# Kernel optimization log

Measured on AMD Instinct MI355X. Metric: run time of the kernel, lower is better.

Reference implementation:

```python
import jax, jax.numpy as jnp
import numpy as np

B, N_PATTS, D_PATTS, L_PATTS, L_SEQ = 32, 32, 12, 32, 1024
L_OUT = 32
RHO = 1.0
BIG = 1e30  # stands in for +inf at DP boundaries (finite to keep grads clean)


def setup_inputs() -> dict:
    key = jax.random.key(0)
    kx, kp = jax.random.split(key)
    x = jax.random.normal(kx, (B, D_PATTS, L_SEQ), dtype=jnp.float32)
    patts = jax.random.normal(kp, (N_PATTS, D_PATTS, L_PATTS), dtype=jnp.float32)
    return {"x": x, "patts": patts}


def _pairwise_sqdist(x, patts):
    # cost[b,n,i,j] = sum_d (patts[n,d,i] - x[b,d,j])^2, shape [B,N,P,L]
    x2 = jnp.sum(x * x, axis=1)            # [B,L]
    p2 = jnp.sum(patts * patts, axis=1)    # [N,P]
    cross = jnp.einsum('bdl,ndp->bnpl', x, patts)  # [B,N,P,L]
    return p2[None, :, :, None] + x2[:, None, None, :] - 2.0 * cross


def _dp_column(a, c, w):
    # Solve cur[i] = c[i] + min(a[i], w*cur[i-1]) sequentially over pattern axis.
    # a, c: [B,N,P]; returns [B,N,P]
    a_t = jnp.moveaxis(a, -1, 0)  # [P,B,N]
    c_t = jnp.moveaxis(c, -1, 0)

    def step(cur_prev, ac):
        a_i, c_i = ac
        cur = c_i + jnp.minimum(a_i, w * cur_prev)
        return cur, cur

    init = jnp.full(c.shape[:-1], BIG, c.dtype)  # no row above the first
    _, cur = jax.lax.scan(step, init, (a_t, c_t))
    return jnp.moveaxis(cur, 0, -1)


def _dtw_dp(cost, w):
    # Weighted DTW recurrence:
    #   D[i,j] = cost[i,j] + min(D[i-1,j-1], w*D[i-1,j], w*D[i,j-1])
    # with D[0,0] = cost[0,0] and out-of-range predecessors = +inf.
    # cost: [B,N,P,L] -> D: [B,N,P,L]
    Bb, Nn, P, L = cost.shape
    cost_t = jnp.moveaxis(cost, -1, 0)  # [L,B,N,P]

    # first column j=0: D[i,0] = c[i,0] + w*D[i-1,0], D[0,0] = c[0,0]
    a0 = jnp.where(jnp.arange(P) == 0, 0.0, BIG).astype(cost.dtype)
    a0 = jnp.broadcast_to(a0, cost.shape[:3])
    d0 = _dp_column(a0, cost_t[0], w)  # [B,N,P]

    def outer_step(d_prev, c_col):
        # prev_shift[i] = D[i-1, j-1]; boundary row is +inf for j >= 1
        top = jnp.full_like(d_prev[..., :1], BIG)
        prev_shift = jnp.concatenate([top, d_prev[..., :-1]], axis=-1)
        a = jnp.minimum(prev_shift, w * d_prev)
        cur = _dp_column(a, c_col, w)
        return cur, cur

    _, rest = jax.lax.scan(outer_step, d0, cost_t[1:])  # [L-1,B,N,P]
    D = jnp.concatenate([d0[None], rest], axis=0)       # [L,B,N,P]
    return jnp.moveaxis(D, 0, -1)                       # [B,N,P,L]


def reference(x, patts):
    w = RHO ** (1.0 / L_PATTS)
    cost = _pairwise_sqdist(x, patts)   # [B,N,P,L]
    D = _dtw_dp(cost, w)                # [B,N,P,L]
    return D[..., -L_OUT:]              # [B,N,P,L_OUT]
```

## Files before the change

### kernel.cpp

```cpp
#include <hip/hip_runtime.h>


#define BIGF 1e30f
#define LL   1024
#define LOUT 32

using v4f = __attribute__((ext_vector_type(4))) float;

__device__ __forceinline__ float wshr1z(float v) {
    return __int_as_float(__builtin_amdgcn_update_dpp(
        0, __float_as_int(v), 0x138 , 0xF, 0xF, false));
}

__device__ __forceinline__ float scan_min64(float t, int lane) {
#pragma unroll
    for (int d = 1; d < 64; d <<= 1) {
        float o = __shfl_up(t, (unsigned)d, 64);
        t = (lane >= d) ? fminf(t, o) : t;
    }
    return t;
}
__device__ __forceinline__ float scan_add64(float t, int lane) {
#pragma unroll
    for (int d = 1; d < 64; d <<= 1) {
        float o = __shfl_up(t, (unsigned)d, 64);
        t += (lane >= d) ? o : 0.0f;
    }
    return t;
}

__global__ __launch_bounds__(64, 1)
void dtw_kernel(const float* __restrict__ x, const float* __restrict__ patts,
                float* __restrict__ out) {
    __shared__ float pT[32 * 12];
    __shared__ float p2s[32];

    const int lane = threadIdx.x;
    const bool l0  = (lane == 0);
    const int blk  = blockIdx.x;
    const int b    = blk >> 5, n = blk & 31;
    const float* __restrict__ xb = x + b * (12 * LL);
    const float* __restrict__ pn = patts + n * (12 * 32);

    if (lane < 32) {
        float s2 = 0.f;
#pragma unroll
        for (int d = 0; d < 12; ++d) {
            float v = pn[d * 32 + lane];
            s2 = fmaf(v, v, s2);
            pT[lane * 12 + d] = -2.0f * v;
        }
        p2s[lane] = s2;
    }

    float SX[12][16];
#pragma unroll
    for (int d = 0; d < 12; ++d) {
#pragma unroll
        for (int c = 0; c < 4; ++c) {
            v4f v = *(const v4f*)(xb + d * LL + 16 * lane + 4 * c);
            SX[d][4*c+0] = v.x; SX[d][4*c+1] = v.y;
            SX[d][4*c+2] = v.z; SX[d][4*c+3] = v.w;
        }
    }
    float SX2[16];
#pragma unroll
    for (int k = 0; k < 16; ++k) {
        float a = 0.f;
#pragma unroll
        for (int d = 0; d < 12; ++d) a = fmaf(SX[d][k], SX[d][k], a);
        SX2[k] = a;
    }
#pragma unroll
    for (int d = 0; d < 12; ++d) {
#pragma unroll
        for (int k = 1; k < 16; ++k) SX[d][k] += SX[d][k-1];
        float tot = SX[d][15];
        float ex  = scan_add64(tot, lane) - tot;
#pragma unroll
        for (int k = 0; k < 16; ++k) SX[d][k] += ex;
    }
    {
#pragma unroll
        for (int k = 1; k < 16; ++k) SX2[k] += SX2[k-1];
        float tot = SX2[15];
        float ex  = scan_add64(tot, lane) - tot;
#pragma unroll
        for (int k = 0; k < 16; ++k) SX2[k] += ex;
    }
    float jp1[16];
#pragma unroll
    for (int k = 0; k < 16; ++k) jp1[k] = (float)(16 * lane + k + 1);

    __syncthreads();

    float pv[12], p2u;
#pragma unroll
    for (int d = 0; d < 12; ++d) pv[d] = pT[d];
    p2u = p2s[0];

    float Dp[16];
    {
        float S[16];
#pragma unroll
        for (int k = 0; k < 16; ++k) S[k] = fmaf(p2u, jp1[k], SX2[k]);
#pragma unroll
        for (int d = 0; d < 12; ++d)
#pragma unroll
            for (int k = 0; k < 16; ++k) S[k] = fmaf(pv[d], SX[d][k], S[k]);
#pragma unroll
        for (int k = 0; k < 16; ++k) Dp[k] = S[k];
        if (lane >= 62) {
            float* ob = out + blk * (32 * LOUT) + (lane - 62) * 16;
#pragma unroll
            for (int c = 0; c < 4; ++c) {
                v4f v = {Dp[4*c], Dp[4*c+1], Dp[4*c+2], Dp[4*c+3]};
                *(v4f*)(ob + 4 * c) = v;
            }
        }
    }
#pragma unroll
    for (int d = 0; d < 12; ++d) pv[d] = pT[12 + d];
    p2u = p2s[1];

#pragma unroll 1
    for (int i = 1; i < 32; ++i) {
        const int ip = (i + 1 < 32) ? i + 1 : 31;
        float pvn[12], p2n;
#pragma unroll
        for (int d = 0; d < 12; ++d) pvn[d] = pT[ip * 12 + d];
        p2n = p2s[ip];

        float S[16];
#pragma unroll
        for (int k = 0; k < 16; ++k) S[k] = fmaf(p2u, jp1[k], SX2[k]);
#pragma unroll
        for (int d = 0; d < 12; ++d)
#pragma unroll
            for (int k = 0; k < 16; ++k) S[k] = fmaf(pv[d], SX[d][k], S[k]);

        float dsh = wshr1z(Dp[15]); dsh = l0 ? BIGF : dsh;
        float se  = wshr1z(S[15]);

        float m[16];
        m[0] = fminf(dsh, Dp[0]) - se;
#pragma unroll
        for (int k = 1; k < 16; ++k) {
            float a = fminf(Dp[k-1], Dp[k]);
            m[k] = fminf(m[k-1], a - S[k-1]);
        }
        float t  = scan_min64(m[15], lane);
        float te = wshr1z(t); te = l0 ? BIGF : te;
#pragma unroll
        for (int k = 0; k < 16; ++k) Dp[k] = S[k] + fminf(te, m[k]);

        if (lane >= 62) {
            float* ob = out + blk * (32 * LOUT) + (lane - 62) * 16;
#pragma unroll
            for (int c = 0; c < 4; ++c) {
                v4f v = {Dp[4*c], Dp[4*c+1], Dp[4*c+2], Dp[4*c+3]};
                *(v4f*)(ob + i * 32 + 4 * c) = v;
            }
        }
#pragma unroll
        for (int d = 0; d < 12; ++d) pv[d] = pvn[d];
        p2u = p2n;
    }
}

extern "C" void kernel_launch(void* const* d_in, const int* in_sizes, int n_in,
                              void* d_out, int out_size, void* d_ws, size_t ws_size,
                              hipStream_t stream) {
    const float* x     = (const float*)d_in[0];
    const float* patts = (const float*)d_in[1];
    float* out         = (float*)d_out;
    dtw_kernel<<<dim3(1024), dim3(64), 0, stream>>>(x, patts, out);
}
```

Before: 85.95 us.

## Use DPP row scan for wave min-scan and software-pipeline next row cost

Replaces the shfl_up-based 64-lane min prefix scan with DPP row_shr steps plus readlane fixups across 16-lane rows, avoiding LDS-backed shuffles on the serial critical path. It also computes the next row's cost vector (Sn) right after the scan is issued, so that independent FMA work can fill the latency of the cross-lane scan. The price is extra registers for Sn alongside S and Dp. With a single wave per block, higher register use matters little for occupancy.

```diff
diff --git a/kernel.cpp b/kernel.cpp
--- a/kernel.cpp
+++ b/kernel.cpp
@@ -7,19 +7,31 @@
 
 using v4f = __attribute__((ext_vector_type(4))) float;
 
+template<int CTRL>
+__device__ __forceinline__ float dpp_self(float v) {
+    return __int_as_float(__builtin_amdgcn_update_dpp(
+        __float_as_int(v), __float_as_int(v), CTRL, 0xF, 0xF, false));
+}
 __device__ __forceinline__ float wshr1z(float v) {
     return __int_as_float(__builtin_amdgcn_update_dpp(
         0, __float_as_int(v), 0x138 , 0xF, 0xF, false));
 }
+__device__ __forceinline__ float rdlane(float v, int l) {
+    return __int_as_float(__builtin_amdgcn_readlane(__float_as_int(v), l));
+}
 
-__device__ __forceinline__ float scan_min64(float t, int lane) {
-#pragma unroll
-    for (int d = 1; d < 64; d <<= 1) {
-        float o = __shfl_up(t, (unsigned)d, 64);
-        t = (lane >= d) ? fminf(t, o) : t;
-    }
+__device__ __forceinline__ float scan_min64_fast(float t, int lane) {
+    t = fminf(t, dpp_self<0x111>(t));
+    t = fminf(t, dpp_self<0x112>(t));
+    t = fminf(t, dpp_self<0x114>(t));
+    t = fminf(t, dpp_self<0x118>(t));
+    float r0 = rdlane(t, 15), r1 = rdlane(t, 31), r2 = rdlane(t, 47);
+    t = fminf(t, (lane >= 16) ? r0 : BIGF);
+    t = fminf(t, (lane >= 32) ? r1 : BIGF);
+    t = fminf(t, (lane >= 48) ? r2 : BIGF);
     return t;
 }
+
 __device__ __forceinline__ float scan_add64(float t, int lane) {
 #pragma unroll
     for (int d = 1; d < 64; d <<= 1) {
@@ -99,45 +111,41 @@
     for (int d = 0; d < 12; ++d) pv[d] = pT[d];
     p2u = p2s[0];
 
-    float Dp[16];
-    {
-        float S[16];
+    float S[16], Dp[16];
 #pragma unroll
-        for (int k = 0; k < 16; ++k) S[k] = fmaf(p2u, jp1[k], SX2[k]);
+    for (int k = 0; k < 16; ++k) S[k] = fmaf(p2u, jp1[k], SX2[k]);
 #pragma unroll
-        for (int d = 0; d < 12; ++d)
+    for (int d = 0; d < 12; ++d)
 #pragma unroll
-            for (int k = 0; k < 16; ++k) S[k] = fmaf(pv[d], SX[d][k], S[k]);
+        for (int k = 0; k < 16; ++k) S[k] = fmaf(pv[d], SX[d][k], S[k]);
 #pragma unroll
-        for (int k = 0; k < 16; ++k) Dp[k] = S[k];
-        if (lane >= 62) {
-            float* ob = out + blk * (32 * LOUT) + (lane - 62) * 16;
+    for (int k = 0; k < 16; ++k) Dp[k] = S[k];
+    if (lane >= 62) {
+        float* ob = out + blk * (32 * LOUT) + (lane - 62) * 16;
 #pragma unroll
-            for (int c = 0; c < 4; ++c) {
-                v4f v = {Dp[4*c], Dp[4*c+1], Dp[4*c+2], Dp[4*c+3]};
-                *(v4f*)(ob + 4 * c) = v;
-            }
+        for (int c = 0; c < 4; ++c) {
+            v4f v = {Dp[4*c], Dp[4*c+1], Dp[4*c+2], Dp[4*c+3]};
+            *(v4f*)(ob + 4 * c) = v;
         }
     }
+
 #pragma unroll
     for (int d = 0; d < 12; ++d) pv[d] = pT[12 + d];
     p2u = p2s[1];
+#pragma unroll
+    for (int k = 0; k < 16; ++k) S[k] = fmaf(p2u, jp1[k], SX2[k]);
+#pragma unroll
+    for (int d = 0; d < 12; ++d)
+#pragma unroll
+        for (int k = 0; k < 16; ++k) S[k] = fmaf(pv[d], SX[d][k], S[k]);
 
 #pragma unroll 1
     for (int i = 1; i < 32; ++i) {
         const int ip = (i + 1 < 32) ? i + 1 : 31;
-        float pvn[12], p2n;
+        float pvn[12];
 #pragma unroll
         for (int d = 0; d < 12; ++d) pvn[d] = pT[ip * 12 + d];
-        p2n = p2s[ip];
-
-        float S[16];
-#pragma unroll
-        for (int k = 0; k < 16; ++k) S[k] = fmaf(p2u, jp1[k], SX2[k]);
-#pragma unroll
-        for (int d = 0; d < 12; ++d)
-#pragma unroll
-            for (int k = 0; k < 16; ++k) S[k] = fmaf(pv[d], SX[d][k], S[k]);
+        float p2n = p2s[ip];
 
         float dsh = wshr1z(Dp[15]); dsh = l0 ? BIGF : dsh;
         float se  = wshr1z(S[15]);
@@ -145,11 +153,19 @@
         float m[16];
         m[0] = fminf(dsh, Dp[0]) - se;
 #pragma unroll
-        for (int k = 1; k < 16; ++k) {
-            float a = fminf(Dp[k-1], Dp[k]);
-            m[k] = fminf(m[k-1], a - S[k-1]);
-        }
-        float t  = scan_min64(m[15], lane);
+        for (int k = 1; k < 16; ++k)
+            m[k] = fminf(m[k-1], fminf(Dp[k-1], Dp[k]) - S[k-1]);
+
+        float t = scan_min64_fast(m[15], lane);
+
+        float Sn[16];
+#pragma unroll
+        for (int k = 0; k < 16; ++k) Sn[k] = fmaf(p2n, jp1[k], SX2[k]);
+#pragma unroll
+        for (int d = 0; d < 12; ++d)
+#pragma unroll
+            for (int k = 0; k < 16; ++k) Sn[k] = fmaf(pvn[d], SX[d][k], Sn[k]);
+
         float te = wshr1z(t); te = l0 ? BIGF : te;
 #pragma unroll
         for (int k = 0; k < 16; ++k) Dp[k] = S[k] + fminf(te, m[k]);
@@ -163,8 +179,7 @@
             }
         }
 #pragma unroll
-        for (int d = 0; d < 12; ++d) pv[d] = pvn[d];
-        p2u = p2n;
+        for (int k = 0; k < 16; ++k) S[k] = Sn[k];
     }
 }
 
```

Result: faster. 81.34 us (-5.4%).
